# Kernel tuning notes

Measured on AMD Instinct MI355X. Metric: run time of the kernel, lower is better.

## Reference

```python
import jax, jax.numpy as jnp
import numpy as np

B, Ng, C, H, W, Nt, M, P = 4, 8192, 256, 128, 128, 512, 8, 4
Ch = C // M  # 32 channels per head
EPS = 1e-5


def setup_inputs():
    key = jax.random.key(0)
    ks = jax.random.split(key, 12)
    s = 0.02
    def w(k, shape):
        return jax.random.normal(k, shape, jnp.float32) * s
    return {
        "query": jax.random.normal(ks[0], (B, Ng, C), jnp.float32),
        "value": jax.random.normal(ks[1], (B, C, H, W), jnp.float32),
        "reference_points": jax.random.uniform(ks[2], (B, Ng, 2), dtype=jnp.float32),
        "trajectory_points": jax.random.uniform(ks[3], (B, Nt, 2), dtype=jnp.float32),
        "in_proj_w": w(ks[4], (3 * C, C)),
        "in_proj_b": jnp.zeros((3 * C,), jnp.float32),
        "mha_out_w": w(ks[5], (C, C)),
        "mha_out_b": jnp.zeros((C,), jnp.float32),
        "ln_g": jnp.ones((C,), jnp.float32),
        "ln_b": jnp.zeros((C,), jnp.float32),
        "traj_w": w(ks[6], (C, 2)),
        "traj_b": jnp.zeros((C,), jnp.float32),
        "offs_w": w(ks[7], (M * P * 2, C)),
        "offs_b": jnp.zeros((M * P * 2,), jnp.float32),
        "attw_w": w(ks[8], (M * P, C)),
        "attw_b": jnp.zeros((M * P,), jnp.float32),
        "out_w": w(ks[9], (C, C)),
        "out_b": jnp.zeros((C,), jnp.float32),
    }


def _bilinear_sample(imgf, x, y):
    # imgf: (NM, Ch, H*W); x, y: (NM, Lq, P) unnormalized pixel coords
    # grid_sample semantics: bilinear, padding_mode='zeros', align_corners=False
    NM = imgf.shape[0]
    Lq, Pp = x.shape[1], x.shape[2]
    x0 = jnp.floor(x); y0 = jnp.floor(y)
    x1 = x0 + 1.0;     y1 = y0 + 1.0

    def gather(xi, yi):
        valid = (xi >= 0) & (xi < W) & (yi >= 0) & (yi < H)
        xc = jnp.clip(xi, 0, W - 1).astype(jnp.int32)
        yc = jnp.clip(yi, 0, H - 1).astype(jnp.int32)
        idx = (yc * W + xc).reshape(NM, 1, Lq * Pp)
        v = jnp.take_along_axis(imgf, jnp.broadcast_to(idx, (NM, Ch, Lq * Pp)), axis=2)
        return v.reshape(NM, Ch, Lq, Pp), valid.astype(imgf.dtype)

    v00, m00 = gather(x0, y0)
    v01, m01 = gather(x1, y0)
    v10, m10 = gather(x0, y1)
    v11, m11 = gather(x1, y1)
    wx1 = x - x0; wx0 = 1.0 - wx1
    wy1 = y - y0; wy0 = 1.0 - wy1
    out = (v00 * (wx0 * wy0 * m00)[:, None]
         + v01 * (wx1 * wy0 * m01)[:, None]
         + v10 * (wx0 * wy1 * m10)[:, None]
         + v11 * (wx1 * wy1 * m11)[:, None])
    return out  # (NM, Ch, Lq, P)


def reference(query, value, reference_points, trajectory_points,
              in_proj_w, in_proj_b, mha_out_w, mha_out_b, ln_g, ln_b,
              traj_w, traj_b, offs_w, offs_b, attw_w, attw_b, out_w, out_b):
    # trajectory projection: (B,Nt,2) -> (B,Nt,C)
    tf = trajectory_points @ traj_w.T + traj_b

    # guidance cross-attention (nn.MultiheadAttention, eval mode => no dropout)
    wq, wk, wv = jnp.split(in_proj_w, 3, axis=0)
    bq, bk, bv = jnp.split(in_proj_b, 3, axis=0)
    q = (query @ wq.T + bq).reshape(B, Ng, M, Ch)
    k = (tf @ wk.T + bk).reshape(B, Nt, M, Ch)
    v = (tf @ wv.T + bv).reshape(B, Nt, M, Ch)
    scores = jnp.einsum('bqmc,bkmc->bmqk', q, k) / jnp.sqrt(jnp.float32(Ch))
    probs = jax.nn.softmax(scores, axis=-1)
    ctx = jnp.einsum('bmqk,bkmc->bqmc', probs, v).reshape(B, Ng, C)
    ctx = ctx @ mha_out_w.T + mha_out_b

    # residual + LayerNorm
    x = query + ctx
    mu = x.mean(-1, keepdims=True)
    var = ((x - mu) ** 2).mean(-1, keepdims=True)
    gq = (x - mu) / jnp.sqrt(var + EPS) * ln_g + ln_b

    # sampling offsets & softmax attention weights (L=1 level)
    offs = (gq @ offs_w.T + offs_b).reshape(B, Ng, M, 1, P, 2)
    aw = jax.nn.softmax((gq @ attw_w.T + attw_b).reshape(B, Ng, M, P), axis=-1)
    loc = reference_points[:, :, None, None, None, :] + offs  # (B,Ng,M,1,P,2)

    # deformable sampling core (single level)
    grid = 2.0 * loc[:, :, :, 0] - 1.0                   # (B,Ng,M,P,2)
    grid = grid.transpose(0, 2, 1, 3, 4).reshape(B * M, Ng, P, 2)
    gx = (grid[..., 0] + 1.0) * (W * 0.5) - 0.5
    gy = (grid[..., 1] + 1.0) * (H * 0.5) - 0.5
    imgf = value.reshape(B * M, Ch, H * W)               # per-head feature maps
    samp = _bilinear_sample(imgf, gx, gy)                # (B*M,Ch,Ng,P)
    w_att = aw.transpose(0, 2, 1, 3).reshape(B * M, 1, Ng, P)
    out = (samp * w_att).sum(-1)                         # (B*M,Ch,Ng)

    # faithful to source: view(B,M,Ch,Ng).transpose(1,2).contiguous().view(B,Ng,C)
    out = out.reshape(B, M, Ch, Ng).transpose(0, 2, 1, 3).reshape(B, Ng, C)
    return out @ out_w.T + out_b
```

## Files before the change

### kernel.cpp

```cpp
#include <hip/hip_runtime.h>
#include <hip/hip_bf16.h>
#include <stdint.h>

typedef __bf16 bf16_t;
typedef __bf16 bf16x8 __attribute__((ext_vector_type(8)));
typedef __bf16 bf16x4 __attribute__((ext_vector_type(4)));
typedef float f32x4 __attribute__((ext_vector_type(4)));

#define CEXP 0.25506807186679906f

__device__ __forceinline__ float ldf(const void* p, size_t i, int isf) {
  return isf ? ((const float*)p)[i] : (float)((const bf16_t*)p)[i];
}

__device__ __forceinline__ int detect_isf(const void* q) {
  const uint16_t* u = (const uint16_t*)q;
  const int lane = threadIdx.x & 63;
  const uint16_t v = u[2 * lane];
  const int e = (v >> 7) & 0xFF;
  const int weird = (e >= 0x86 || (v != 0 && e <= 0x65)) ? 1 : 0;
  return (__popcll(__ballot(weird)) >= 16) ? 1 : 0;
}

__device__ __forceinline__ float fexp2(float x) {
#if __has_builtin(__builtin_amdgcn_exp2f)
  return __builtin_amdgcn_exp2f(x);
#else
  return exp2f(x);
#endif
}

__device__ __forceinline__ f32x4 mfma16x16x16(bf16x4 a, bf16x4 b, f32x4 c) {
#if __has_builtin(__builtin_amdgcn_mfma_f32_16x16x16_bf16)
  return __builtin_amdgcn_mfma_f32_16x16x16_bf16(a, b, c, 0, 0, 0);
#else
  typedef short s16x4 __attribute__((ext_vector_type(4)));
  return __builtin_amdgcn_mfma_f32_16x16x16bf16_1k(
      __builtin_bit_cast(s16x4, a), __builtin_bit_cast(s16x4, b), c, 0, 0, 0);
#endif
}

__device__ __forceinline__ void stage16(const bf16_t* g, bf16_t* l) {
  __builtin_amdgcn_global_load_lds((const __attribute__((address_space(1))) void*)g,
                                   (__attribute__((address_space(3))) void*)l, 16, 0, 0);
}

__global__ __launch_bounds__(256) void prep_all(
    const void* __restrict__ query,
    const void* in_w, const void* in_b, const void* mow, const void* mob,
    const void* outw, const void* outb,
    const void* trajp, const void* tw, const void* tb,
    const void* offs_w, const void* attw_w, const void* offs_b, const void* attw_b,
    bf16_t* __restrict__ blob, bf16_t* __restrict__ tf,
    bf16_t* __restrict__ Wph, bf16_t* __restrict__ Wpl, bf16_t* __restrict__ bp)
{
  const int isf = detect_isf(query);
  const int bid = blockIdx.x;
  if (bid < 322) {
    const int g = (bid * 256 + threadIdx.x) * 4;
    if (g >= 328960) return;
    const void* src; size_t off;
    if      (g < 196608) { src = in_w; off = g; }
    else if (g < 197376) { src = in_b; off = g - 196608; }
    else if (g < 262912) { src = mow;  off = g - 197376; }
    else if (g < 263168) { src = mob;  off = g - 262912; }
    else if (g < 328704) { src = outw; off = g - 263168; }
    else                 { src = outb; off = g - 328704; }
#pragma unroll
    for (int k = 0; k < 4; k++) blob[g + k] = (bf16_t)ldf(src, off + k, isf);
  } else if (bid < 322 + 2048) {
    const int rowb = bid - 322;
    const int c = threadIdx.x;
    const float x = ldf(trajp, rowb * 2 + 0, isf);
    const float y = ldf(trajp, rowb * 2 + 1, isf);
    const float v = x * ldf(tw, c * 2 + 0, isf) + y * ldf(tw, c * 2 + 1, isf) + ldf(tb, c, isf);
    tf[(size_t)rowb * 256 + c] = (bf16_t)v;
  } else {
    const int idx = (bid - 2370) * 256 + threadIdx.x;
    const int rowp = idx >> 8, c = idx & 255;
    float v = 0.0f;
    if (rowp < 64)      v = ldf(offs_w, rowp * 256 + c, isf);
    else if (rowp < 96) v = ldf(attw_w, (rowp - 64) * 256 + c, isf);
    const bf16_t hi = (bf16_t)v;
    Wph[idx] = hi;
    Wpl[idx] = (bf16_t)(v - (float)hi);
    if (idx < 128) {
      float bv = 0.0f;
      if (idx < 64)      bv = ldf(offs_b, idx, isf);
      else if (idx < 96) bv = ldf(attw_b, idx - 64, isf);
      bp[idx] = (bf16_t)bv;
    }
  }
}

#define TM 128
#define TN 128
#define TKK 64

__global__ __launch_bounds__(256) void gemm_async(
    const bf16_t* __restrict__ A, const bf16_t* __restrict__ W,
    const bf16_t* __restrict__ bias, void* __restrict__ Cout,
    void* __restrict__ Cout2, int Ndim, int Kdim, int mode, float kscale,
    const void* __restrict__ qdet)
{
  __shared__ __align__(16) bf16_t As[TM * TKK];
  __shared__ __align__(16) bf16_t Ws[TN * TKK];
  const int t    = threadIdx.x;
  const int lane = t & 63;
  const int w    = t >> 6;
  const int wm   = (w & 1) * 64;
  const int wn   = (w >> 1) * 64;
  const int q4   = lane >> 4;
  const int r16  = lane & 15;
  const int tm   = blockIdx.x * TM;
  const int tn   = blockIdx.y * TN;

  f32x4 acc[4][4] = {};

  for (int kt = 0; kt < Kdim; kt += TKK) {
    __syncthreads();
#pragma unroll
    for (int r = 0; r < 4; r++) {
      const int L = w * 256 + r * 64 + lane;
      const int R = L >> 3, c = (L & 7) * 8;
      stage16(A + (size_t)(tm + R) * Kdim + kt + c, As + L * 8);
      stage16(W + (size_t)(tn + R) * Kdim + kt + c, Ws + L * 8);
    }
    __syncthreads();
#pragma unroll
    for (int ks = 0; ks < TKK; ks += 32) {
      bf16x8 af[4], bfm[4];
#pragma unroll
      for (int i = 0; i < 4; i++)
        af[i] = *(const bf16x8*)(As + (wm + 16 * i + r16) * TKK + ks + q4 * 8);
#pragma unroll
      for (int j = 0; j < 4; j++)
        bfm[j] = *(const bf16x8*)(Ws + (wn + 16 * j + r16) * TKK + ks + q4 * 8);
#pragma unroll
      for (int i = 0; i < 4; i++)
#pragma unroll
        for (int j = 0; j < 4; j++)
          acc[i][j] = __builtin_amdgcn_mfma_f32_16x16x32_bf16(af[i], bfm[j], acc[i][j], 0, 0, 0);
    }
  }

  const int isf = (mode == 3) ? detect_isf(qdet) : 1;
#pragma unroll
  for (int j = 0; j < 4; j++) {
    const int col = tn + wn + 16 * j + r16;
    const float bv = (float)bias[col];
#pragma unroll
    for (int i = 0; i < 4; i++) {
      const int row0 = tm + wm + 16 * i + q4 * 4;
#pragma unroll
      for (int rr = 0; rr < 4; rr++) {
        const float v = acc[i][j][rr] + bv;
        const size_t off = (size_t)(row0 + rr) * Ndim + col;
        if (mode == 0) {
          ((bf16_t*)Cout)[off] = (bf16_t)v;
        } else if (mode == 6) {
          const int rowg = row0 + rr;
          if (col < 256) {
            ((bf16_t*)Cout)[(size_t)rowg * 256 + col] = (bf16_t)(v * kscale);
          } else {
            const int bb = rowg >> 9, tt = rowg & 511;
            const int c2 = col - 256;
            const int mm = c2 >> 5, ch = c2 & 31;
            ((bf16_t*)Cout2)[(((size_t)(bb * 8 + mm) * 32 + ch) << 9) + tt] = (bf16_t)v;
          }
        } else {
          if (isf) ((float*)Cout)[off] = v; else ((bf16_t*)Cout)[off] = (bf16_t)v;
        }
      }
    }
  }
}

__global__ __launch_bounds__(256) void gemm_f32a(
    const void* __restrict__ Araw, const bf16_t* __restrict__ W,
    const bf16_t* __restrict__ bias, bf16_t* __restrict__ Cout,
    int Ndim, int Kdim, const void* __restrict__ qdet)
{
  __shared__ __align__(16) bf16_t As[TM * TKK];
  __shared__ __align__(16) bf16_t Ws[TN * TKK];
  const int t    = threadIdx.x;
  const int lane = t & 63;
  const int w    = t >> 6;
  const int wm   = (w & 1) * 64;
  const int wn   = (w >> 1) * 64;
  const int q4   = lane >> 4;
  const int r16  = lane & 15;
  const int tm   = blockIdx.x * TM;
  const int tn   = blockIdx.y * TN;
  const int aisf = detect_isf(qdet);

  f32x4 acc[4][4] = {};
  const int srow = t >> 1;
  const int skb  = (t & 1) * 32;

  for (int kt = 0; kt < Kdim; kt += TKK) {
    __syncthreads();
    if (aisf) {
      const float4* ga = (const float4*)((const float*)Araw + (size_t)(tm + srow) * Kdim + kt + skb);
#pragma unroll
      for (int kk = 0; kk < 8; kk++) {
        const float4 u = ga[kk];
        bf16x4 h = {(bf16_t)u.x, (bf16_t)u.y, (bf16_t)u.z, (bf16_t)u.w};
        *(bf16x4*)(As + srow * TKK + skb + kk * 4) = h;
      }
    } else {
      const uint4* ga = (const uint4*)((const bf16_t*)Araw + (size_t)(tm + srow) * Kdim + kt + skb);
      uint4* la = (uint4*)(As + srow * TKK + skb);
      la[0] = ga[0]; la[1] = ga[1]; la[2] = ga[2]; la[3] = ga[3];
    }
    {
      const uint4* gw = (const uint4*)(W + (size_t)(tn + srow) * Kdim + kt + skb);
      uint4* lw = (uint4*)(Ws + srow * TKK + skb);
      lw[0] = gw[0]; lw[1] = gw[1]; lw[2] = gw[2]; lw[3] = gw[3];
    }
    __syncthreads();
#pragma unroll
    for (int ks = 0; ks < TKK; ks += 32) {
      bf16x8 af[4], bfm[4];
#pragma unroll
      for (int i = 0; i < 4; i++)
        af[i] = *(const bf16x8*)(As + (wm + 16 * i + r16) * TKK + ks + q4 * 8);
#pragma unroll
      for (int j = 0; j < 4; j++)
        bfm[j] = *(const bf16x8*)(Ws + (wn + 16 * j + r16) * TKK + ks + q4 * 8);
#pragma unroll
      for (int i = 0; i < 4; i++)
#pragma unroll
        for (int j = 0; j < 4; j++)
          acc[i][j] = __builtin_amdgcn_mfma_f32_16x16x32_bf16(af[i], bfm[j], acc[i][j], 0, 0, 0);
    }
  }

#pragma unroll
  for (int j = 0; j < 4; j++) {
    const int col = tn + wn + 16 * j + r16;
    const float bv = (float)bias[col];
#pragma unroll
    for (int i = 0; i < 4; i++) {
      const int row0 = tm + wm + 16 * i + q4 * 4;
#pragma unroll
      for (int rr = 0; rr < 4; rr++)
        Cout[(size_t)(row0 + rr) * Ndim + col] = (bf16_t)(acc[i][j][rr] + bv);
    }
  }
}

__global__ __launch_bounds__(256, 2) void attn_kernel(
    const bf16_t* __restrict__ Q, const bf16_t* __restrict__ Kk,
    const bf16_t* __restrict__ Vt, bf16_t* __restrict__ ctx)
{
  const int t = threadIdx.x;
  const int lane = t & 63, w = t >> 6;
  const int q4 = lane >> 4, r16 = lane & 15;
  const int bm = blockIdx.y;
  const int b = bm >> 3, m = bm & 7;
  const int q0 = blockIdx.x * 512 + w * 128;

  bf16x8 qf[8];
#pragma unroll
  for (int qt = 0; qt < 8; qt++)
    qf[qt] = *(const bf16x8*)(Q + ((size_t)(b * 8192 + q0 + qt * 16 + r16) * 256 + m * 32 + q4 * 8));

  f32x4 acc[8][2] = {};
  float lsum[8] = {0.f, 0.f, 0.f, 0.f, 0.f, 0.f, 0.f, 0.f};

  const bf16_t* kbase  = Kk + (size_t)b * 512 * 256 + m * 32 + (size_t)r16 * 256 + q4 * 8;
  const bf16_t* vbase0 = Vt + (size_t)bm * 32 * 512 + ((size_t)r16 << 9) + q4 * 4;
  const bf16_t* vbase1 = vbase0 + (16 << 9);

  bf16x8 kf = *(const bf16x8*)(kbase);
  bf16x4 v0 = *(const bf16x4*)(vbase0);
  bf16x4 v1 = *(const bf16x4*)(vbase1);

  for (int k0 = 0; k0 < 512; k0 += 16) {
    const int nxt = k0 + 16;
    const bf16x8 kf_n = *(const bf16x8*)(kbase + (size_t)nxt * 256);
    const bf16x4 v0_n = *(const bf16x4*)(vbase0 + nxt);
    const bf16x4 v1_n = *(const bf16x4*)(vbase1 + nxt);
#pragma unroll
    for (int qt = 0; qt < 8; qt++) {
      f32x4 z = {};
      const f32x4 s = __builtin_amdgcn_mfma_f32_16x16x32_bf16(kf, qf[qt], z, 0, 0, 0);
      union { float f; uint32_t u; } a0, a1, a2, a3;
      a0.f = fexp2(s[0]); a1.f = fexp2(s[1]); a2.f = fexp2(s[2]); a3.f = fexp2(s[3]);
      lsum[qt] += (a0.f + a1.f) + (a2.f + a3.f);
      uint2 rp;
      rp.x = __builtin_amdgcn_perm(a1.u + 0x8000u, a0.u + 0x8000u, 0x07060302u);
      rp.y = __builtin_amdgcn_perm(a3.u + 0x8000u, a2.u + 0x8000u, 0x07060302u);
      const bf16x4 p = __builtin_bit_cast(bf16x4, rp);
      acc[qt][0] = mfma16x16x16(v0, p, acc[qt][0]);
      acc[qt][1] = mfma16x16x16(v1, p, acc[qt][1]);
    }
    kf = kf_n; v0 = v0_n; v1 = v1_n;
  }

#pragma unroll
  for (int qt = 0; qt < 8; qt++) {
    float v = lsum[qt];
    v += __shfl_xor(v, 16, 64);
    v += __shfl_xor(v, 32, 64);
    const float inv = 1.0f / v;
    const size_t row = (size_t)b * 8192 + q0 + qt * 16 + r16;
    bf16x4 o0, o1;
#pragma unroll
    for (int rr = 0; rr < 4; rr++) {
      o0[rr] = (bf16_t)(acc[qt][0][rr] * inv);
      o1[rr] = (bf16_t)(acc[qt][1][rr] * inv);
    }
    *(bf16x4*)(ctx + row * 256 + m * 32 + q4 * 4)      = o0;
    *(bf16x4*)(ctx + row * 256 + m * 32 + 16 + q4 * 4) = o1;
  }
}

__global__ __launch_bounds__(256) void ln_kernel(
    const bf16_t* __restrict__ y2, const void* __restrict__ query,
    const void* __restrict__ g, const void* __restrict__ beta,
    bf16_t* __restrict__ gqh, bf16_t* __restrict__ gql)
{
  const int isf = detect_isf(query);
  const int rowb = blockIdx.x * 4 + (threadIdx.x >> 6);
  const int lane = threadIdx.x & 63;
  const size_t base = (size_t)rowb * 256;
  float x[4];
  float s = 0.f;
#pragma unroll
  for (int k = 0; k < 4; k++) {
    const int c = lane + 64 * k;
    x[k] = ldf(query, base + c, isf) + (float)y2[base + c];
    s += x[k];
  }
  for (int d = 1; d < 64; d <<= 1) s += __shfl_xor(s, d, 64);
  const float mu = s * (1.0f / 256.0f);
  float vs = 0.f;
#pragma unroll
  for (int k = 0; k < 4; k++) { const float d = x[k] - mu; vs += d * d; }
  for (int d = 1; d < 64; d <<= 1) vs += __shfl_xor(vs, d, 64);
  const float rstd = rsqrtf(vs * (1.0f / 256.0f) + 1e-5f);
#pragma unroll
  for (int k = 0; k < 4; k++) {
    const int c = lane + 64 * k;
    const float gv = (x[k] - mu) * rstd * ldf(g, c, isf) + ldf(beta, c, isf);
    const bf16_t hi = (bf16_t)gv;
    gqh[base + c] = hi;
    gql[base + c] = (bf16_t)(gv - (float)hi);
  }
}

__global__ __launch_bounds__(256) void gemm_offs(
    const bf16_t* __restrict__ Ahg, const bf16_t* __restrict__ Alg,
    const bf16_t* __restrict__ Whg, const bf16_t* __restrict__ Wlg,
    const bf16_t* __restrict__ bias, float* __restrict__ Cout)
{
  __shared__ __align__(16) bf16_t Ah[128 * 64];
  __shared__ __align__(16) bf16_t Al[128 * 64];
  __shared__ __align__(16) bf16_t Wh[128 * 64];
  __shared__ __align__(16) bf16_t Wl[128 * 64];
  const int t    = threadIdx.x;
  const int lane = t & 63;
  const int w    = t >> 6;
  const int wm   = (w & 1) * 64;
  const int wn   = (w >> 1) * 64;
  const int q4   = lane >> 4;
  const int r16  = lane & 15;
  const int tm   = blockIdx.x * 128;

  f32x4 acc[4][4] = {};
  const int srow = t >> 1;
  const int skb  = (t & 1) * 32;

  for (int kt = 0; kt < 256; kt += 64) {
    __syncthreads();
    {
      const uint4* g0 = (const uint4*)(Ahg + (size_t)(tm + srow) * 256 + kt + skb);
      uint4* l0 = (uint4*)(Ah + srow * 64 + skb);
      l0[0] = g0[0]; l0[1] = g0[1]; l0[2] = g0[2]; l0[3] = g0[3];
      const uint4* g1 = (const uint4*)(Alg + (size_t)(tm + srow) * 256 + kt + skb);
      uint4* l1 = (uint4*)(Al + srow * 64 + skb);
      l1[0] = g1[0]; l1[1] = g1[1]; l1[2] = g1[2]; l1[3] = g1[3];
      const uint4* g2 = (const uint4*)(Whg + (size_t)srow * 256 + kt + skb);
      uint4* l2 = (uint4*)(Wh + srow * 64 + skb);
      l2[0] = g2[0]; l2[1] = g2[1]; l2[2] = g2[2]; l2[3] = g2[3];
      const uint4* g3 = (const uint4*)(Wlg + (size_t)srow * 256 + kt + skb);
      uint4* l3 = (uint4*)(Wl + srow * 64 + skb);
      l3[0] = g3[0]; l3[1] = g3[1]; l3[2] = g3[2]; l3[3] = g3[3];
    }
    __syncthreads();
#pragma unroll
    for (int ks = 0; ks < 64; ks += 32) {
      bf16x8 ah[4], al[4], bh[4], bl[4];
#pragma unroll
      for (int i = 0; i < 4; i++) {
        ah[i] = *(const bf16x8*)(Ah + (wm + 16 * i + r16) * 64 + ks + q4 * 8);
        al[i] = *(const bf16x8*)(Al + (wm + 16 * i + r16) * 64 + ks + q4 * 8);
      }
#pragma unroll
      for (int j = 0; j < 4; j++) {
        bh[j] = *(const bf16x8*)(Wh + (wn + 16 * j + r16) * 64 + ks + q4 * 8);
        bl[j] = *(const bf16x8*)(Wl + (wn + 16 * j + r16) * 64 + ks + q4 * 8);
      }
#pragma unroll
      for (int i = 0; i < 4; i++)
#pragma unroll
        for (int j = 0; j < 4; j++) {
          f32x4 a = acc[i][j];
          a = __builtin_amdgcn_mfma_f32_16x16x32_bf16(al[i], bh[j], a, 0, 0, 0);
          a = __builtin_amdgcn_mfma_f32_16x16x32_bf16(ah[i], bl[j], a, 0, 0, 0);
          a = __builtin_amdgcn_mfma_f32_16x16x32_bf16(ah[i], bh[j], a, 0, 0, 0);
          acc[i][j] = a;
        }
    }
  }

#pragma unroll
  for (int j = 0; j < 4; j++) {
    const int col = wn + 16 * j + r16;
    const float bv = (float)bias[col];
#pragma unroll
    for (int i = 0; i < 4; i++) {
      const int row0 = tm + wm + 16 * i + q4 * 4;
#pragma unroll
      for (int rr = 0; rr < 4; rr++)
        Cout[(size_t)(row0 + rr) * 128 + col] = acc[i][j][rr] + bv;
    }
  }
}

__global__ __launch_bounds__(256) void transpose_value(
    const void* __restrict__ V, bf16_t* __restrict__ Vp, const void* __restrict__ qdet)
{
  __shared__ bf16_t tile[32][130];
  const int isf = detect_isf(qdet);
  const int bid = blockIdx.x;
  const int h = bid & 127;
  const int bm = bid >> 7;
  const int b = bm >> 3, mm = bm & 7;
  const int t = threadIdx.x;
  for (int idx = t; idx < 32 * 128; idx += 256) {
    const int ch = idx >> 7, ww = idx & 127;
    tile[ch][ww] = (bf16_t)ldf(V, (((size_t)b * 256 + mm * 32 + ch) * 128 + h) * 128 + ww, isf);
  }
  __syncthreads();
  const size_t base = ((size_t)bm * 128 + h) * 4096;
  for (int idx = t; idx < 32 * 128; idx += 256) {
    const int ww = idx >> 5, ch = idx & 31;
    Vp[base + idx] = tile[ch][ww];
  }
}

__global__ __launch_bounds__(256) void sampler(
    const float* __restrict__ ys, const void* __restrict__ refp,
    const bf16_t* __restrict__ vperm, bf16_t* __restrict__ outs,
    const void* __restrict__ qdet)
{
  const int isf = detect_isf(qdet);
  const int t = threadIdx.x;
  const int qt = blockIdx.x;
  const int bm = blockIdx.y;
  const int b = bm >> 3, m = bm & 7;
  const int qq = qt * 256 + t;
  const size_t row = (size_t)b * 8192 + qq;
  const float* y = ys + row * 128;
  const float rx = ldf(refp, row * 2 + 0, isf);
  const float ry = ldf(refp, row * 2 + 1, isf);

  const float l0 = y[64 + m * 4 + 0], l1 = y[64 + m * 4 + 1];
  const float l2 = y[64 + m * 4 + 2], l3 = y[64 + m * 4 + 3];
  const float mx = fmaxf(fmaxf(l0, l1), fmaxf(l2, l3));
  const float e0 = __expf(l0 - mx), e1 = __expf(l1 - mx);
  const float e2 = __expf(l2 - mx), e3 = __expf(l3 - mx);
  const float inv = 1.0f / (e0 + e1 + e2 + e3);
  const float aw[4] = {e0 * inv, e1 * inv, e2 * inv, e3 * inv};

  float acc[32];
#pragma unroll
  for (int ch = 0; ch < 32; ch++) acc[ch] = 0.0f;

  const bf16_t* vbase = vperm + (size_t)bm * (128 * 128 * 32);

  for (int p = 0; p < 4; p++) {
    const float gx = (rx + y[m * 8 + p * 2 + 0]) * 128.0f - 0.5f;
    const float gy = (ry + y[m * 8 + p * 2 + 1]) * 128.0f - 0.5f;
    const float x0f = floorf(gx), y0f = floorf(gy);
    const int x0 = (int)x0f, y0i = (int)y0f;
    const float wx1 = gx - x0f, wx0 = 1.0f - wx1;
    const float wy1 = gy - y0f, wy0 = 1.0f - wy1;
    const float a = aw[p];
    for (int cy = 0; cy < 2; cy++) {
      const int yy = y0i + cy;
      if (yy < 0 || yy >= 128) continue;
      const float wy = cy ? wy1 : wy0;
      for (int cx = 0; cx < 2; cx++) {
        const int xx = x0 + cx;
        if (xx < 0 || xx >= 128) continue;
        const float wgt = a * wy * (cx ? wx1 : wx0);
        const bf16x8* src8 = (const bf16x8*)(vbase + ((size_t)yy * 128 + xx) * 32);
#pragma unroll
        for (int vv = 0; vv < 4; vv++) {
          const bf16x8 d = src8[vv];
#pragma unroll
          for (int e = 0; e < 8; e++) acc[vv * 8 + e] += wgt * (float)d[e];
        }
      }
    }
  }

  const size_t obase = (size_t)b * 8192;
#pragma unroll
  for (int ch = 0; ch < 32; ch++) {
    const size_t orow = obase + (size_t)(ch * 8 + m) * 32 + qt;
    outs[orow * 256 + t] = (bf16_t)acc[ch];
  }
}

extern "C" void kernel_launch(void* const* d_in, const int* in_sizes, int n_in,
                              void* d_out, int out_size, void* d_ws, size_t ws_size,
                              hipStream_t stream) {
  const void* query = d_in[0];
  const void* value = d_in[1];
  const void* refp  = d_in[2];
  const void* trajp = d_in[3];
  const void* in_w  = d_in[4];
  const void* in_b  = d_in[5];
  const void* mow   = d_in[6];
  const void* mob   = d_in[7];
  const void* lng   = d_in[8];
  const void* lnb   = d_in[9];
  const void* tw    = d_in[10];
  const void* tb    = d_in[11];
  const void* ow    = d_in[12];
  const void* ob    = d_in[13];
  const void* aww   = d_in[14];
  const void* awb   = d_in[15];
  const void* outw  = d_in[16];
  const void* outb  = d_in[17];

  char* base = (char*)d_ws;
  float*  ysamp = (float*)(base);
  bf16_t* qout  = (bf16_t*)(base + 16777216);
  bf16_t* ctx   = (bf16_t*)(base + 33554432);
  bf16_t* y2    = (bf16_t*)(base + 50331648);
  bf16_t* tf_ws = (bf16_t*)(base + 67108864);
  bf16_t* k_ws  = (bf16_t*)(base + 68157440);
  bf16_t* vt_g  = (bf16_t*)(base + 69206016);
  bf16_t* blob  = (bf16_t*)(base + 70254592);

  bf16_t* gqh   = qout;
  bf16_t* gql   = ctx;
  bf16_t* vperm = (bf16_t*)(base + 16777216);
  bf16_t* outs  = y2;

  bf16_t* inw_bf  = blob;
  bf16_t* inb_bf  = blob + 196608;
  bf16_t* mow_bf  = blob + 197376;
  bf16_t* mob_bf  = blob + 262912;
  bf16_t* outw_bf = blob + 263168;
  bf16_t* outb_bf = blob + 328704;
  bf16_t* wph     = blob + 328960;
  bf16_t* wpl     = blob + 361728;
  bf16_t* bpad    = blob + 394496;

  prep_all<<<dim3(2498), dim3(256), 0, stream>>>(
      query, in_w, in_b, mow, mob, outw, outb, trajp, tw, tb,
      ow, aww, ob, awb, blob, tf_ws, wph, wpl, bpad);
  gemm_async<<<dim3(16, 4), dim3(256), 0, stream>>>(
      tf_ws, inw_bf + 65536, inb_bf + 256, (void*)k_ws, (void*)vt_g, 512, 256, 6, CEXP, query);
  gemm_f32a<<<dim3(256, 2), dim3(256), 0, stream>>>(
      query, inw_bf, inb_bf, qout, 256, 256, query);
  attn_kernel<<<dim3(16, 32), dim3(256), 0, stream>>>(qout, k_ws, vt_g, ctx);
  gemm_async<<<dim3(256, 2), dim3(256), 0, stream>>>(
      ctx, mow_bf, mob_bf, (void*)y2, nullptr, 256, 256, 0, 1.0f, query);
  ln_kernel<<<dim3(8192), dim3(256), 0, stream>>>(y2, query, lng, lnb, gqh, gql);
  gemm_offs<<<dim3(256, 1), dim3(256), 0, stream>>>(gqh, gql, wph, wpl, bpad, ysamp);
  transpose_value<<<dim3(4096), dim3(256), 0, stream>>>(value, vperm, query);
  sampler<<<dim3(32, 32), dim3(256), 0, stream>>>(ysamp, refp, vperm, outs, query);
  gemm_async<<<dim3(256, 2), dim3(256), 0, stream>>>(
      outs, outw_bf, outb_bf, d_out, nullptr, 256, 256, 3, 1.0f, query);
}
```

Measured before the change: 357.2 us.

## Halve attention tile per wave, vectorize layernorm and value transpose

The attention kernel now handles 64 queries per wave instead of 128. The grid doubles and launch bounds allow 4 blocks per SM, which cuts register use and aims to raise occupancy across the 256 CUs; the cost is that each K/V fragment is loaded twice as often. The manual round-to-bf16 perm trick is replaced by plain casts. The layernorm and value-transpose kernels switch from scalar strided accesses to 4- and 8-wide vector loads and stores to improve memory efficiency, with the transpose tile padding changed to 136.

New measurement: 360.5 us. About the same (+0.9%).

```diff
diff --git a/kernel.cpp b/kernel.cpp
--- a/kernel.cpp
+++ b/kernel.cpp
@@ -250,7 +250,7 @@
   }
 }
 
-__global__ __launch_bounds__(256, 2) void attn_kernel(
+__global__ __launch_bounds__(256, 4) void attn_kernel(
     const bf16_t* __restrict__ Q, const bf16_t* __restrict__ Kk,
     const bf16_t* __restrict__ Vt, bf16_t* __restrict__ ctx)
 {
@@ -259,15 +259,15 @@
   const int q4 = lane >> 4, r16 = lane & 15;
   const int bm = blockIdx.y;
   const int b = bm >> 3, m = bm & 7;
-  const int q0 = blockIdx.x * 512 + w * 128;
-
-  bf16x8 qf[8];
-#pragma unroll
-  for (int qt = 0; qt < 8; qt++)
+  const int q0 = blockIdx.x * 256 + w * 64;
+
+  bf16x8 qf[4];
+#pragma unroll
+  for (int qt = 0; qt < 4; qt++)
     qf[qt] = *(const bf16x8*)(Q + ((size_t)(b * 8192 + q0 + qt * 16 + r16) * 256 + m * 32 + q4 * 8));
 
-  f32x4 acc[8][2] = {};
-  float lsum[8] = {0.f, 0.f, 0.f, 0.f, 0.f, 0.f, 0.f, 0.f};
+  f32x4 acc[4][2] = {};
+  float lsum[4] = {0.f, 0.f, 0.f, 0.f};
 
   const bf16_t* kbase  = Kk + (size_t)b * 512 * 256 + m * 32 + (size_t)r16 * 256 + q4 * 8;
   const bf16_t* vbase0 = Vt + (size_t)bm * 32 * 512 + ((size_t)r16 << 9) + q4 * 4;
@@ -283,16 +283,13 @@
     const bf16x4 v0_n = *(const bf16x4*)(vbase0 + nxt);
     const bf16x4 v1_n = *(const bf16x4*)(vbase1 + nxt);
 #pragma unroll
-    for (int qt = 0; qt < 8; qt++) {
+    for (int qt = 0; qt < 4; qt++) {
       f32x4 z = {};
       const f32x4 s = __builtin_amdgcn_mfma_f32_16x16x32_bf16(kf, qf[qt], z, 0, 0, 0);
-      union { float f; uint32_t u; } a0, a1, a2, a3;
-      a0.f = fexp2(s[0]); a1.f = fexp2(s[1]); a2.f = fexp2(s[2]); a3.f = fexp2(s[3]);
-      lsum[qt] += (a0.f + a1.f) + (a2.f + a3.f);
-      uint2 rp;
-      rp.x = __builtin_amdgcn_perm(a1.u + 0x8000u, a0.u + 0x8000u, 0x07060302u);
-      rp.y = __builtin_amdgcn_perm(a3.u + 0x8000u, a2.u + 0x8000u, 0x07060302u);
-      const bf16x4 p = __builtin_bit_cast(bf16x4, rp);
+      const float e0 = fexp2(s[0]), e1 = fexp2(s[1]);
+      const float e2 = fexp2(s[2]), e3 = fexp2(s[3]);
+      lsum[qt] += (e0 + e1) + (e2 + e3);
+      const bf16x4 p = {(bf16_t)e0, (bf16_t)e1, (bf16_t)e2, (bf16_t)e3};
       acc[qt][0] = mfma16x16x16(v0, p, acc[qt][0]);
       acc[qt][1] = mfma16x16x16(v1, p, acc[qt][1]);
     }
@@ -300,7 +297,7 @@
   }
 
 #pragma unroll
-  for (int qt = 0; qt < 8; qt++) {
+  for (int qt = 0; qt < 4; qt++) {
     float v = lsum[qt];
     v += __shfl_xor(v, 16, 64);
     v += __shfl_xor(v, 32, 64);
@@ -326,14 +323,21 @@
   const int rowb = blockIdx.x * 4 + (threadIdx.x >> 6);
   const int lane = threadIdx.x & 63;
   const size_t base = (size_t)rowb * 256;
+  const int c0 = lane * 4;
   float x[4];
-  float s = 0.f;
-#pragma unroll
-  for (int k = 0; k < 4; k++) {
-    const int c = lane + 64 * k;
-    x[k] = ldf(query, base + c, isf) + (float)y2[base + c];
-    s += x[k];
-  }
+  {
+    const bf16x4 yv = *(const bf16x4*)(y2 + base + c0);
+    if (isf) {
+      const float4 qv = *(const float4*)((const float*)query + base + c0);
+      x[0] = qv.x + (float)yv[0]; x[1] = qv.y + (float)yv[1];
+      x[2] = qv.z + (float)yv[2]; x[3] = qv.w + (float)yv[3];
+    } else {
+      const bf16x4 qv = *(const bf16x4*)((const bf16_t*)query + base + c0);
+#pragma unroll
+      for (int k = 0; k < 4; k++) x[k] = (float)qv[k] + (float)yv[k];
+    }
+  }
+  float s = x[0] + x[1] + x[2] + x[3];
   for (int d = 1; d < 64; d <<= 1) s += __shfl_xor(s, d, 64);
   const float mu = s * (1.0f / 256.0f);
   float vs = 0.f;
@@ -341,14 +345,28 @@
   for (int k = 0; k < 4; k++) { const float d = x[k] - mu; vs += d * d; }
   for (int d = 1; d < 64; d <<= 1) vs += __shfl_xor(vs, d, 64);
   const float rstd = rsqrtf(vs * (1.0f / 256.0f) + 1e-5f);
+  float gw[4], bb[4];
+  if (isf) {
+    const float4 gg = *(const float4*)((const float*)g + c0);
+    const float4 bv = *(const float4*)((const float*)beta + c0);
+    gw[0] = gg.x; gw[1] = gg.y; gw[2] = gg.z; gw[3] = gg.w;
+    bb[0] = bv.x; bb[1] = bv.y; bb[2] = bv.z; bb[3] = bv.w;
+  } else {
+    const bf16x4 gg = *(const bf16x4*)((const bf16_t*)g + c0);
+    const bf16x4 bv = *(const bf16x4*)((const bf16_t*)beta + c0);
+#pragma unroll
+    for (int k = 0; k < 4; k++) { gw[k] = (float)gg[k]; bb[k] = (float)bv[k]; }
+  }
+  bf16x4 hi4, lo4;
 #pragma unroll
   for (int k = 0; k < 4; k++) {
-    const int c = lane + 64 * k;
-    const float gv = (x[k] - mu) * rstd * ldf(g, c, isf) + ldf(beta, c, isf);
+    const float gv = (x[k] - mu) * rstd * gw[k] + bb[k];
     const bf16_t hi = (bf16_t)gv;
-    gqh[base + c] = hi;
-    gql[base + c] = (bf16_t)(gv - (float)hi);
-  }
+    hi4[k] = hi;
+    lo4[k] = (bf16_t)(gv - (float)hi);
+  }
+  *(bf16x4*)(gqh + base + c0) = hi4;
+  *(bf16x4*)(gql + base + c0) = lo4;
 }
 
 __global__ __launch_bounds__(256) void gemm_offs(
@@ -433,23 +451,42 @@
 __global__ __launch_bounds__(256) void transpose_value(
     const void* __restrict__ V, bf16_t* __restrict__ Vp, const void* __restrict__ qdet)
 {
-  __shared__ bf16_t tile[32][130];
+  __shared__ __align__(16) bf16_t tile[32][136];
   const int isf = detect_isf(qdet);
   const int bid = blockIdx.x;
   const int h = bid & 127;
   const int bm = bid >> 7;
   const int b = bm >> 3, mm = bm & 7;
   const int t = threadIdx.x;
-  for (int idx = t; idx < 32 * 128; idx += 256) {
-    const int ch = idx >> 7, ww = idx & 127;
-    tile[ch][ww] = (bf16_t)ldf(V, (((size_t)b * 256 + mm * 32 + ch) * 128 + h) * 128 + ww, isf);
+  const int ch  = t >> 3;
+  const int ww0 = (t & 7) * 16;
+  const size_t ibase = (((size_t)b * 256 + mm * 32 + ch) * 128 + h) * 128 + ww0;
+  if (isf) {
+    const float4* src = (const float4*)((const float*)V + ibase);
+    bf16x8 h0, h1;
+#pragma unroll
+    for (int k = 0; k < 2; k++) {
+      const float4 u0 = src[k * 2], u1 = src[k * 2 + 1];
+      bf16x8 hh = {(bf16_t)u0.x, (bf16_t)u0.y, (bf16_t)u0.z, (bf16_t)u0.w,
+                   (bf16_t)u1.x, (bf16_t)u1.y, (bf16_t)u1.z, (bf16_t)u1.w};
+      if (k == 0) h0 = hh; else h1 = hh;
+    }
+    *(bf16x8*)(&tile[ch][ww0])     = h0;
+    *(bf16x8*)(&tile[ch][ww0 + 8]) = h1;
+  } else {
+    const bf16x8* src = (const bf16x8*)((const bf16_t*)V + ibase);
+    *(bf16x8*)(&tile[ch][ww0])     = src[0];
+    *(bf16x8*)(&tile[ch][ww0 + 8]) = src[1];
   }
   __syncthreads();
   const size_t base = ((size_t)bm * 128 + h) * 4096;
-  for (int idx = t; idx < 32 * 128; idx += 256) {
-    const int ww = idx >> 5, ch = idx & 31;
-    Vp[base + idx] = tile[ch][ww];
-  }
+  const int ww = t >> 1;
+  const int c0 = (t & 1) * 16;
+  bf16x8 o0, o1;
+#pragma unroll
+  for (int e = 0; e < 8; e++) { o0[e] = tile[c0 + e][ww]; o1[e] = tile[c0 + 8 + e][ww]; }
+  *(bf16x8*)(Vp + base + ww * 32 + c0)     = o0;
+  *(bf16x8*)(Vp + base + ww * 32 + c0 + 8) = o1;
 }
 
 __global__ __launch_bounds__(256) void sampler(
@@ -571,7 +608,7 @@
       tf_ws, inw_bf + 65536, inb_bf + 256, (void*)k_ws, (void*)vt_g, 512, 256, 6, CEXP, query);
   gemm_f32a<<<dim3(256, 2), dim3(256), 0, stream>>>(
       query, inw_bf, inb_bf, qout, 256, 256, query);
-  attn_kernel<<<dim3(16, 32), dim3(256), 0, stream>>>(qout, k_ws, vt_g, ctx);
+  attn_kernel<<<dim3(32, 32), dim3(256), 0, stream>>>(qout, k_ws, vt_g, ctx);
   gemm_async<<<dim3(256, 2), dim3(256), 0, stream>>>(
       ctx, mow_bf, mob_bf, (void*)y2, nullptr, 256, 256, 0, 1.0f, query);
   ln_kernel<<<dim3(8192), dim3(256), 0, stream>>>(y2, query, lng, lnb, gqh, gql);
```
